# Optimization experiments

Measured on AMD Instinct MI355X. Metric: run time of the kernel, lower is better.

The kernel has to match this reference:

```python
import jax, jax.numpy as jnp
import numpy as np

DIM = 192
NUM_HEADS = 6
WIN = (2, 7, 7)


def _relative_position_index(win):
    d, h, w = win
    coords = np.stack(np.meshgrid(np.arange(d), np.arange(h), np.arange(w), indexing='ij'))
    cf = coords.reshape(3, -1)  # (3, n)
    rel = cf[:, :, None] - cf[:, None, :]  # (3, n, n)
    rel = rel.transpose(1, 2, 0).copy()
    rel[:, :, 0] += d - 1
    rel[:, :, 1] += h - 1
    rel[:, :, 2] += w - 1
    rel[:, :, 0] *= (2 * h - 1) * (2 * w - 1)
    rel[:, :, 1] *= 2 * w - 1
    return rel.sum(-1).astype(np.int32)  # (n, n)


def setup_inputs() -> dict:
    key = jax.random.key(0)
    ks = jax.random.split(key, 8)
    n = WIN[0] * WIN[1] * WIN[2]  # 98
    table_size = (2 * WIN[0] - 1) * (2 * WIN[1] - 1) * (2 * WIN[2] - 1)  # 507
    b_ = 4096
    nW = 64
    x = jax.random.normal(ks[0], (b_, n, DIM), dtype=jnp.float32)
    mask = jax.random.normal(ks[1], (nW, n, n), dtype=jnp.float32)
    qkv_w = jax.random.normal(ks[2], (3 * DIM, DIM), dtype=jnp.float32) * (DIM ** -0.5)
    qkv_b = jnp.zeros((3 * DIM,), dtype=jnp.float32)
    proj_w = jax.random.normal(ks[3], (DIM, DIM), dtype=jnp.float32) * (DIM ** -0.5)
    proj_b = jnp.zeros((DIM,), dtype=jnp.float32)
    rpb_table = jax.random.normal(ks[4], (table_size, NUM_HEADS), dtype=jnp.float32) * 0.02
    rel_idx = jnp.asarray(_relative_position_index(WIN))  # (n, n) int32
    return {"x": x, "mask": mask, "qkv_w": qkv_w, "qkv_b": qkv_b,
            "proj_w": proj_w, "proj_b": proj_b, "rpb_table": rpb_table,
            "rel_idx": rel_idx}


def reference(x, mask, qkv_w, qkv_b, proj_w, proj_b, rpb_table, rel_idx):
    b_, n, c = x.shape
    H = NUM_HEADS
    hd = c // H
    scale = hd ** -0.5
    # QKV projection: (b_, n, 3, H, hd) -> (3, b_, H, n, hd)
    qkv = (x @ qkv_w.T + qkv_b).reshape(b_, n, 3, H, hd).transpose(2, 0, 3, 1, 4)
    q, k, v = qkv[0] * scale, qkv[1], qkv[2]
    attn = jnp.einsum('bhnd,bhmd->bhnm', q, k)
    # relative position bias gathered per (n, n) pair -> (H, n, n)
    bias = rpb_table[rel_idx]  # (n, n, H)
    attn = attn + bias.transpose(2, 0, 1)[None]
    # window mask add
    nW = mask.shape[0]
    attn = attn.reshape(b_ // nW, nW, H, n, n) + mask[None, :, None]
    attn = attn.reshape(b_, H, n, n)
    attn = jax.nn.softmax(attn, axis=-1)
    out = jnp.einsum('bhnm,bhmd->bhnd', attn, v)
    out = out.transpose(0, 2, 1, 3).reshape(b_, n, c)
    return out @ proj_w.T + proj_b
```

## Files before the change

### kernel.cpp

```cpp
#include <hip/hip_runtime.h>
#include <hip/hip_bf16.h>

#define NN 98
#define CC 192
#define NH 6
#define HDIM 32
#define NWIN 64
#define MPAD 100
#define NSTR 200
#define SWS 1920

typedef float f32x4 __attribute__((ext_vector_type(4)));
typedef __bf16 bf16x8 __attribute__((ext_vector_type(8)));
typedef __bf16 bf16x4 __attribute__((ext_vector_type(4)));

__device__ __forceinline__ f32x4 mfma_bf16(bf16x8 a, bf16x8 b, f32x4 c) {
  return __builtin_amdgcn_mfma_f32_16x16x32_bf16(a, b, c, 0, 0, 0);
}

__device__ __forceinline__ bf16x8 zero8() {
  bf16x8 z;
#pragma unroll
  for (int i = 0; i < 8; ++i) z[i] = (__bf16)0.0f;
  return z;
}

__device__ __forceinline__ bf16x8 ldw8(const float* __restrict__ p) {
  f32x4 a = *(const f32x4*)p;
  f32x4 b = *(const f32x4*)(p + 4);
  bf16x8 r;
  r[0] = (__bf16)a[0]; r[1] = (__bf16)a[1]; r[2] = (__bf16)a[2]; r[3] = (__bf16)a[3];
  r[4] = (__bf16)b[0]; r[5] = (__bf16)b[1]; r[6] = (__bf16)b[2]; r[7] = (__bf16)b[3];
  return r;
}

__device__ __forceinline__ bf16x8 ldlds8(const __bf16* p, int row, int k0) {
  int rc = row < NN ? row : (NN - 1);
  bf16x8 v = *(const bf16x8*)(p + rc * NSTR + k0);
  if (row >= NN) v = zero8();
  return v;
}

__global__ void prep_kernel(const float* __restrict__ mask,
                            const float* __restrict__ rpb,
                            const int* __restrict__ rel_idx,
                            float* __restrict__ biasp,
                            float* __restrict__ maskp) {
  int i = blockIdx.x * 256 + threadIdx.x;
  if (i < NH * NN * MPAD) {
    int m = i % MPAD;
    int rem = i / MPAD;
    int n = rem % NN;
    int h = rem / NN;
    biasp[i] = (m < NN) ? rpb[rel_idx[n * NN + m] * NH + h] : -1e30f;
  }
  if (i < NWIN * NN * MPAD) {
    int m = i % MPAD;
    int rem = i / MPAD;
    int n = rem % NN;
    int wi = rem / NN;
    maskp[i] = (m < NN) ? mask[(wi * NN + n) * NN + m] : -1e30f;
  }
}

__global__ __launch_bounds__(384, 3) void attn_kernel(
    const float* __restrict__ x,
    const float* __restrict__ qkv_w,
    const float* __restrict__ qkv_b,
    const float* __restrict__ proj_w,
    const float* __restrict__ proj_b,
    const float* __restrict__ biasp,
    const float* __restrict__ maskp,
    float* __restrict__ out) {
  __shared__ alignas(16) __bf16 xs[NN * NSTR];
  __shared__ alignas(16) __bf16 stage[NH * SWS];

  const int b = blockIdx.x;
  const int tid = threadIdx.x;
  const int w = tid >> 6;
  const int lane = tid & 63;
  const int l15 = lane & 15;
  const int quad = lane >> 4;
  __bf16* st = stage + w * SWS;

  const float* xb = x + (size_t)b * (NN * CC);
  for (int i = tid; i < NN * CC / 4; i += 384) {
    int e = i * 4;
    int n = e / CC;
    int c = e - n * CC;
    f32x4 v = *(const f32x4*)(xb + e);
    bf16x4 p;
    p[0] = (__bf16)v[0]; p[1] = (__bf16)v[1]; p[2] = (__bf16)v[2]; p[3] = (__bf16)v[3];
    *(bf16x4*)&xs[n * NSTR + c] = p;
  }
  __syncthreads();

  f32x4 accA[4][7];
#pragma unroll
  for (int ct = 0; ct < 2; ++ct) {
    float bk = qkv_b[CC + w * HDIM + ct * 16 + l15];
    float bv = qkv_b[2 * CC + w * HDIM + ct * 16 + l15];
#pragma unroll
    for (int rt = 0; rt < 7; ++rt) {
      f32x4 tk = {bk, bk, bk, bk};
      f32x4 tv = {bv, bv, bv, bv};
      accA[ct][rt] = tk;
      accA[2 + ct][rt] = tv;
    }
  }
#pragma unroll
  for (int ks = 0; ks < 6; ++ks) {
    const int k0 = ks * 32 + quad * 8;
    bf16x8 b0 = ldw8(qkv_w + (size_t)(CC + w * HDIM + l15) * CC + k0);
    bf16x8 b1 = ldw8(qkv_w + (size_t)(CC + w * HDIM + 16 + l15) * CC + k0);
    bf16x8 b2 = ldw8(qkv_w + (size_t)(2 * CC + w * HDIM + l15) * CC + k0);
    bf16x8 b3 = ldw8(qkv_w + (size_t)(2 * CC + w * HDIM + 16 + l15) * CC + k0);
#pragma unroll
    for (int rt = 0; rt < 7; ++rt) {
      bf16x8 a = ldlds8(xs, rt * 16 + l15, k0);
      accA[0][rt] = mfma_bf16(a, b0, accA[0][rt]);
      accA[1][rt] = mfma_bf16(a, b1, accA[1][rt]);
      accA[2][rt] = mfma_bf16(a, b2, accA[2][rt]);
      accA[3][rt] = mfma_bf16(a, b3, accA[3][rt]);
    }
  }

  bf16x8 ka[7];
#pragma unroll
  for (int rt = 0; rt < 7; ++rt) {
#pragma unroll
    for (int ct = 0; ct < 2; ++ct) {
      f32x4 v = accA[ct][rt];
      int hd = ct * 16 + l15;
#pragma unroll
      for (int r = 0; r < 4; ++r) st[(quad * 4 + r) * 40 + hd] = (__bf16)v[r];
    }
    bf16x8 f = *(const bf16x8*)&st[l15 * 40 + quad * 8];
    if (rt * 16 + l15 >= NN) f = zero8();
    ka[rt] = f;
  }

  bf16x8 va[2][4];
#pragma unroll
  for (int ks = 0; ks < 4; ++ks) {
#pragma unroll
    for (int h2 = 0; h2 < 2; ++h2) {
      int rt = 2 * ks + h2;
      if (rt < 7) {
#pragma unroll
        for (int ct = 0; ct < 2; ++ct) {
          f32x4 v = accA[2 + ct][rt];
          int d = ct * 16 + l15;
          int mloc = h2 * 16 + quad * 4;
          bf16x4 p;
#pragma unroll
          for (int r = 0; r < 4; ++r) p[r] = (__bf16)v[r];
          *(bf16x4*)&st[d * 40 + mloc] = p;
        }
      }
    }
#pragma unroll
    for (int dt = 0; dt < 2; ++dt) {
      bf16x8 f = *(const bf16x8*)&st[(dt * 16 + l15) * 40 + quad * 8];
      if (ks == 3 && quad >= 2) f = zero8();
      va[dt][ks] = f;
    }
  }

  f32x4 accB[2][7];
#pragma unroll
  for (int ct = 0; ct < 2; ++ct) {
    float bq = qkv_b[w * HDIM + ct * 16 + l15];
#pragma unroll
    for (int rt = 0; rt < 7; ++rt) {
      f32x4 t = {bq, bq, bq, bq};
      accB[ct][rt] = t;
    }
  }
#pragma unroll
  for (int ks = 0; ks < 6; ++ks) {
    const int k0 = ks * 32 + quad * 8;
    bf16x8 b0 = ldw8(qkv_w + (size_t)(w * HDIM + l15) * CC + k0);
    bf16x8 b1 = ldw8(qkv_w + (size_t)(w * HDIM + 16 + l15) * CC + k0);
#pragma unroll
    for (int rt = 0; rt < 7; ++rt) {
      bf16x8 a = ldlds8(xs, rt * 16 + l15, k0);
      accB[0][rt] = mfma_bf16(a, b0, accB[0][rt]);
      accB[1][rt] = mfma_bf16(a, b1, accB[1][rt]);
    }
  }

  const float scale = 0.17677669529663687f;
  bf16x8 qb[7];
#pragma unroll
  for (int rt = 0; rt < 7; ++rt) {
#pragma unroll
    for (int ct = 0; ct < 2; ++ct) {
      f32x4 v = accB[ct][rt];
      int hd = ct * 16 + l15;
#pragma unroll
      for (int r = 0; r < 4; ++r) st[(quad * 4 + r) * 40 + hd] = (__bf16)(v[r] * scale);
    }
    bf16x8 f = *(const bf16x8*)&st[l15 * 40 + quad * 8];
    if (rt * 16 + l15 >= NN) f = zero8();
    qb[rt] = f;
  }

  __syncthreads();
  __bf16* O_lds = xs;

  const int wmask = b & (NWIN - 1);
#pragma unroll 1
  for (int nb = 0; nb < 7; ++nb) {
    f32x4 sacc[7];
    const f32x4 z4 = {0.f, 0.f, 0.f, 0.f};
#pragma unroll
    for (int mt = 0; mt < 7; ++mt) sacc[mt] = mfma_bf16(ka[mt], qb[nb], z4);

    int n = nb * 16 + l15;
    bool nvalid = (n < NN);
    int nc = nvalid ? n : 0;
    const float* bp = biasp + (size_t)(w * NN + nc) * MPAD;
    const float* mp = maskp + (size_t)(wmask * NN + nc) * MPAD;

    float sv[28];
    float mx = -3.0e38f;
#pragma unroll
    for (int mt = 0; mt < 7; ++mt) {
      int m0 = mt * 16 + quad * 4;
      f32x4 add = z4;
      bool ld = nvalid && (m0 < MPAD);
      if (ld) {
        f32x4 bm = *(const f32x4*)(bp + m0);
        f32x4 mm = *(const f32x4*)(mp + m0);
        add = bm + mm;
      }
#pragma unroll
      for (int r = 0; r < 4; ++r) {
        float v = ld ? (sacc[mt][r] + add[r]) : -1e30f;
        sv[mt * 4 + r] = v;
        mx = fmaxf(mx, v);
      }
    }
    mx = fmaxf(mx, __shfl_xor(mx, 16, 64));
    mx = fmaxf(mx, __shfl_xor(mx, 32, 64));
    float sum = 0.f;
#pragma unroll
    for (int i = 0; i < 28; ++i) {
      float p = __expf(sv[i] - mx);
      sv[i] = p;
      sum += p;
    }
    sum += __shfl_xor(sum, 16, 64);
    sum += __shfl_xor(sum, 32, 64);
    float rinv = 1.0f / sum;

#pragma unroll
    for (int mt = 0; mt < 7; ++mt) {
      bf16x4 p;
#pragma unroll
      for (int r = 0; r < 4; ++r) p[r] = (__bf16)sv[mt * 4 + r];
      *(bf16x4*)&st[l15 * 120 + mt * 16 + quad * 4] = p;
    }
    bf16x8 pf[4];
#pragma unroll
    for (int ks = 0; ks < 4; ++ks) {
      bf16x8 f = *(const bf16x8*)&st[l15 * 120 + ks * 32 + quad * 8];
      if (ks == 3 && quad >= 2) f = zero8();
      pf[ks] = f;
    }

#pragma unroll
    for (int dt = 0; dt < 2; ++dt) {
      f32x4 o = z4;
#pragma unroll
      for (int ks = 0; ks < 4; ++ks) o = mfma_bf16(va[dt][ks], pf[ks], o);
      if (nvalid) {
        bf16x4 p;
#pragma unroll
        for (int r = 0; r < 4; ++r) p[r] = (__bf16)(o[r] * rinv);
        *(bf16x4*)&O_lds[n * NSTR + w * HDIM + dt * 16 + quad * 4] = p;
      }
    }
  }
  __syncthreads();

  f32x4 accP[2][7];
#pragma unroll
  for (int ct = 0; ct < 2; ++ct) {
    float pb = proj_b[w * HDIM + ct * 16 + l15];
#pragma unroll
    for (int rt = 0; rt < 7; ++rt) {
      f32x4 t = {pb, pb, pb, pb};
      accP[ct][rt] = t;
    }
  }
#pragma unroll
  for (int ks = 0; ks < 6; ++ks) {
    const int k0 = ks * 32 + quad * 8;
    bf16x8 b0 = ldw8(proj_w + (size_t)(w * HDIM + l15) * CC + k0);
    bf16x8 b1 = ldw8(proj_w + (size_t)(w * HDIM + 16 + l15) * CC + k0);
#pragma unroll
    for (int rt = 0; rt < 7; ++rt) {
      bf16x8 a = ldlds8(O_lds, rt * 16 + l15, k0);
      accP[0][rt] = mfma_bf16(a, b0, accP[0][rt]);
      accP[1][rt] = mfma_bf16(a, b1, accP[1][rt]);
    }
  }

  float* ob = out + (size_t)b * (NN * CC);
#pragma unroll
  for (int ct = 0; ct < 2; ++ct) {
    int cout = w * HDIM + ct * 16 + l15;
#pragma unroll
    for (int rt = 0; rt < 7; ++rt) {
      f32x4 v = accP[ct][rt];
#pragma unroll
      for (int r = 0; r < 4; ++r) {
        int n = rt * 16 + quad * 4 + r;
        if (n < NN) ob[n * CC + cout] = v[r];
      }
    }
  }
}

extern "C" void kernel_launch(void* const* d_in, const int* in_sizes, int n_in,
                              void* d_out, int out_size, void* d_ws, size_t ws_size,
                              hipStream_t stream) {
  const float* x = (const float*)d_in[0];
  const float* mask = (const float*)d_in[1];
  const float* qkv_w = (const float*)d_in[2];
  const float* qkv_b = (const float*)d_in[3];
  const float* proj_w = (const float*)d_in[4];
  const float* proj_b = (const float*)d_in[5];
  const float* rpb = (const float*)d_in[6];
  const int* rel_idx = (const int*)d_in[7];

  float* biasp = (float*)d_ws;
  float* maskp = biasp + NH * NN * MPAD;

  int prep_threads = NWIN * NN * MPAD;
  prep_kernel<<<(prep_threads + 255) / 256, 256, 0, stream>>>(mask, rpb, rel_idx, biasp, maskp);
  attn_kernel<<<4096, 384, 0, stream>>>(x, qkv_w, qkv_b, proj_w, proj_b, biasp, maskp,
                                        (float*)d_out);
}
```

Baseline: 1.746 ms.

## Pre-convert weights to bf16 fragment layout, split K/V GEMMs, use exp2 softmax

The prep kernel now converts the QKV and projection weights once into bf16 arrays laid out in MFMA fragment order, so each lane loads one contiguous 16-byte vector instead of two fp32 vectors plus conversions in every block. The K and V projections are computed one after the other with a shared accumulator set, which lowers register pressure. Softmax switches to exp2, with log2(e) folded into the query scale, bias and mask. This adds work and workspace to the prep kernel and reloads the x tile from LDS one extra time.

```diff
diff --git a/kernel.cpp b/kernel.cpp
--- a/kernel.cpp
+++ b/kernel.cpp
@@ -10,6 +10,10 @@
 #define NSTR 200
 #define SWS 1920
 
+#define WKV_ELEMS 73728
+#define WQ_ELEMS  36864
+#define WP_ELEMS  36864
+
 typedef float f32x4 __attribute__((ext_vector_type(4)));
 typedef __bf16 bf16x8 __attribute__((ext_vector_type(8)));
 typedef __bf16 bf16x4 __attribute__((ext_vector_type(4)));
@@ -25,13 +29,12 @@
   return z;
 }
 
-__device__ __forceinline__ bf16x8 ldw8(const float* __restrict__ p) {
-  f32x4 a = *(const f32x4*)p;
-  f32x4 b = *(const f32x4*)(p + 4);
-  bf16x8 r;
-  r[0] = (__bf16)a[0]; r[1] = (__bf16)a[1]; r[2] = (__bf16)a[2]; r[3] = (__bf16)a[3];
-  r[4] = (__bf16)b[0]; r[5] = (__bf16)b[1]; r[6] = (__bf16)b[2]; r[7] = (__bf16)b[3];
-  return r;
+__device__ __forceinline__ float fast_exp2(float x) {
+#if __has_builtin(__builtin_amdgcn_exp2f)
+  return __builtin_amdgcn_exp2f(x);
+#else
+  return exp2f(x);
+#endif
 }
 
 __device__ __forceinline__ bf16x8 ldlds8(const __bf16* p, int row, int k0) {
@@ -44,33 +47,65 @@
 __global__ void prep_kernel(const float* __restrict__ mask,
                             const float* __restrict__ rpb,
                             const int* __restrict__ rel_idx,
+                            const float* __restrict__ qkv_w,
+                            const float* __restrict__ proj_w,
                             float* __restrict__ biasp,
-                            float* __restrict__ maskp) {
+                            float* __restrict__ maskp,
+                            __bf16* __restrict__ wkvp,
+                            __bf16* __restrict__ wqp,
+                            __bf16* __restrict__ wpp) {
+  const float LOG2E = 1.4426950408889634f;
   int i = blockIdx.x * 256 + threadIdx.x;
   if (i < NH * NN * MPAD) {
     int m = i % MPAD;
     int rem = i / MPAD;
     int n = rem % NN;
     int h = rem / NN;
-    biasp[i] = (m < NN) ? rpb[rel_idx[n * NN + m] * NH + h] : -1e30f;
+    biasp[i] = (m < NN) ? rpb[rel_idx[n * NN + m] * NH + h] * LOG2E : -1e30f;
   }
   if (i < NWIN * NN * MPAD) {
     int m = i % MPAD;
     int rem = i / MPAD;
     int n = rem % NN;
     int wi = rem / NN;
-    maskp[i] = (m < NN) ? mask[(wi * NN + n) * NN + m] : -1e30f;
+    maskp[i] = (m < NN) ? mask[(wi * NN + n) * NN + m] * LOG2E : -1e30f;
+  }
+  if (i < WKV_ELEMS) {
+    int j = i & 7;
+    int lane = (i >> 3) & 63;
+    int f = (i >> 9) & 3;
+    int t = i >> 11;
+    int ks = t % 6;
+    int w = t / 6;
+    int l15 = lane & 15, quad = lane >> 4;
+    int row = (f < 2 ? CC : 2 * CC) + w * HDIM + (f & 1) * 16 + l15;
+    int col = ks * 32 + quad * 8 + j;
+    wkvp[i] = (__bf16)qkv_w[row * CC + col];
+  }
+  if (i < WQ_ELEMS) {
+    int j = i & 7;
+    int lane = (i >> 3) & 63;
+    int f = (i >> 9) & 1;
+    int t = i >> 10;
+    int ks = t % 6;
+    int w = t / 6;
+    int l15 = lane & 15, quad = lane >> 4;
+    int row = w * HDIM + f * 16 + l15;
+    int col = ks * 32 + quad * 8 + j;
+    wqp[i] = (__bf16)qkv_w[row * CC + col];
+    wpp[i] = (__bf16)proj_w[row * CC + col];
   }
 }
 
 __global__ __launch_bounds__(384, 3) void attn_kernel(
     const float* __restrict__ x,
-    const float* __restrict__ qkv_w,
     const float* __restrict__ qkv_b,
-    const float* __restrict__ proj_w,
     const float* __restrict__ proj_b,
     const float* __restrict__ biasp,
     const float* __restrict__ maskp,
+    const __bf16* __restrict__ wkvp,
+    const __bf16* __restrict__ wqp,
+    const __bf16* __restrict__ wpp,
     float* __restrict__ out) {
   __shared__ alignas(16) __bf16 xs[NN * NSTR];
   __shared__ alignas(16) __bf16 stage[NH * SWS];
@@ -95,33 +130,27 @@
   }
   __syncthreads();
 
-  f32x4 accA[4][7];
+  f32x4 acc[2][7];
+
 #pragma unroll
   for (int ct = 0; ct < 2; ++ct) {
-    float bk = qkv_b[CC + w * HDIM + ct * 16 + l15];
-    float bv = qkv_b[2 * CC + w * HDIM + ct * 16 + l15];
-#pragma unroll
-    for (int rt = 0; rt < 7; ++rt) {
-      f32x4 tk = {bk, bk, bk, bk};
-      f32x4 tv = {bv, bv, bv, bv};
-      accA[ct][rt] = tk;
-      accA[2 + ct][rt] = tv;
-    }
-  }
-#pragma unroll
-  for (int ks = 0; ks < 6; ++ks) {
-    const int k0 = ks * 32 + quad * 8;
-    bf16x8 b0 = ldw8(qkv_w + (size_t)(CC + w * HDIM + l15) * CC + k0);
-    bf16x8 b1 = ldw8(qkv_w + (size_t)(CC + w * HDIM + 16 + l15) * CC + k0);
-    bf16x8 b2 = ldw8(qkv_w + (size_t)(2 * CC + w * HDIM + l15) * CC + k0);
-    bf16x8 b3 = ldw8(qkv_w + (size_t)(2 * CC + w * HDIM + 16 + l15) * CC + k0);
-#pragma unroll
-    for (int rt = 0; rt < 7; ++rt) {
-      bf16x8 a = ldlds8(xs, rt * 16 + l15, k0);
-      accA[0][rt] = mfma_bf16(a, b0, accA[0][rt]);
-      accA[1][rt] = mfma_bf16(a, b1, accA[1][rt]);
-      accA[2][rt] = mfma_bf16(a, b2, accA[2][rt]);
-      accA[3][rt] = mfma_bf16(a, b3, accA[3][rt]);
+    float bb = qkv_b[CC + w * HDIM + ct * 16 + l15];
+#pragma unroll
+    for (int rt = 0; rt < 7; ++rt) { f32x4 t = {bb, bb, bb, bb}; acc[ct][rt] = t; }
+  }
+  {
+    const __bf16* wb = wkvp + (size_t)(w * 24) * 512 + lane * 8;
+#pragma unroll
+    for (int ks = 0; ks < 6; ++ks) {
+      bf16x8 b0 = *(const bf16x8*)(wb + (ks * 4 + 0) * 512);
+      bf16x8 b1 = *(const bf16x8*)(wb + (ks * 4 + 1) * 512);
+      const int k0 = ks * 32 + quad * 8;
+#pragma unroll
+      for (int rt = 0; rt < 7; ++rt) {
+        bf16x8 a = ldlds8(xs, rt * 16 + l15, k0);
+        acc[0][rt] = mfma_bf16(a, b0, acc[0][rt]);
+        acc[1][rt] = mfma_bf16(a, b1, acc[1][rt]);
+      }
     }
   }
 
@@ -130,7 +159,7 @@
   for (int rt = 0; rt < 7; ++rt) {
 #pragma unroll
     for (int ct = 0; ct < 2; ++ct) {
-      f32x4 v = accA[ct][rt];
+      f32x4 v = acc[ct][rt];
       int hd = ct * 16 + l15;
 #pragma unroll
       for (int r = 0; r < 4; ++r) st[(quad * 4 + r) * 40 + hd] = (__bf16)v[r];
@@ -140,6 +169,28 @@
     ka[rt] = f;
   }
 
+#pragma unroll
+  for (int ct = 0; ct < 2; ++ct) {
+    float bb = qkv_b[2 * CC + w * HDIM + ct * 16 + l15];
+#pragma unroll
+    for (int rt = 0; rt < 7; ++rt) { f32x4 t = {bb, bb, bb, bb}; acc[ct][rt] = t; }
+  }
+  {
+    const __bf16* wb = wkvp + (size_t)(w * 24) * 512 + lane * 8;
+#pragma unroll
+    for (int ks = 0; ks < 6; ++ks) {
+      bf16x8 b0 = *(const bf16x8*)(wb + (ks * 4 + 2) * 512);
+      bf16x8 b1 = *(const bf16x8*)(wb + (ks * 4 + 3) * 512);
+      const int k0 = ks * 32 + quad * 8;
+#pragma unroll
+      for (int rt = 0; rt < 7; ++rt) {
+        bf16x8 a = ldlds8(xs, rt * 16 + l15, k0);
+        acc[0][rt] = mfma_bf16(a, b0, acc[0][rt]);
+        acc[1][rt] = mfma_bf16(a, b1, acc[1][rt]);
+      }
+    }
+  }
+
   bf16x8 va[2][4];
 #pragma unroll
   for (int ks = 0; ks < 4; ++ks) {
@@ -149,7 +200,7 @@
       if (rt < 7) {
 #pragma unroll
         for (int ct = 0; ct < 2; ++ct) {
-          f32x4 v = accA[2 + ct][rt];
+          f32x4 v = acc[ct][rt];
           int d = ct * 16 + l15;
           int mloc = h2 * 16 + quad * 4;
           bf16x4 p;
@@ -167,39 +218,38 @@
     }
   }
 
-  f32x4 accB[2][7];
 #pragma unroll
   for (int ct = 0; ct < 2; ++ct) {
     float bq = qkv_b[w * HDIM + ct * 16 + l15];
 #pragma unroll
-    for (int rt = 0; rt < 7; ++rt) {
-      f32x4 t = {bq, bq, bq, bq};
-      accB[ct][rt] = t;
-    }
-  }
-#pragma unroll
-  for (int ks = 0; ks < 6; ++ks) {
-    const int k0 = ks * 32 + quad * 8;
-    bf16x8 b0 = ldw8(qkv_w + (size_t)(w * HDIM + l15) * CC + k0);
-    bf16x8 b1 = ldw8(qkv_w + (size_t)(w * HDIM + 16 + l15) * CC + k0);
-#pragma unroll
-    for (int rt = 0; rt < 7; ++rt) {
-      bf16x8 a = ldlds8(xs, rt * 16 + l15, k0);
-      accB[0][rt] = mfma_bf16(a, b0, accB[0][rt]);
-      accB[1][rt] = mfma_bf16(a, b1, accB[1][rt]);
-    }
-  }
-
-  const float scale = 0.17677669529663687f;
+    for (int rt = 0; rt < 7; ++rt) { f32x4 t = {bq, bq, bq, bq}; acc[ct][rt] = t; }
+  }
+  {
+    const __bf16* wb = wqp + (size_t)(w * 12) * 512 + lane * 8;
+#pragma unroll
+    for (int ks = 0; ks < 6; ++ks) {
+      bf16x8 b0 = *(const bf16x8*)(wb + (ks * 2 + 0) * 512);
+      bf16x8 b1 = *(const bf16x8*)(wb + (ks * 2 + 1) * 512);
+      const int k0 = ks * 32 + quad * 8;
+#pragma unroll
+      for (int rt = 0; rt < 7; ++rt) {
+        bf16x8 a = ldlds8(xs, rt * 16 + l15, k0);
+        acc[0][rt] = mfma_bf16(a, b0, acc[0][rt]);
+        acc[1][rt] = mfma_bf16(a, b1, acc[1][rt]);
+      }
+    }
+  }
+
+  const float qscale = 0.17677669529663687f * 1.4426950408889634f;
   bf16x8 qb[7];
 #pragma unroll
   for (int rt = 0; rt < 7; ++rt) {
 #pragma unroll
     for (int ct = 0; ct < 2; ++ct) {
-      f32x4 v = accB[ct][rt];
+      f32x4 v = acc[ct][rt];
       int hd = ct * 16 + l15;
 #pragma unroll
-      for (int r = 0; r < 4; ++r) st[(quad * 4 + r) * 40 + hd] = (__bf16)(v[r] * scale);
+      for (int r = 0; r < 4; ++r) st[(quad * 4 + r) * 40 + hd] = (__bf16)(v[r] * qscale);
     }
     bf16x8 f = *(const bf16x8*)&st[l15 * 40 + quad * 8];
     if (rt * 16 + l15 >= NN) f = zero8();
@@ -212,8 +262,8 @@
   const int wmask = b & (NWIN - 1);
 #pragma unroll 1
   for (int nb = 0; nb < 7; ++nb) {
+    const f32x4 z4 = {0.f, 0.f, 0.f, 0.f};
     f32x4 sacc[7];
-    const f32x4 z4 = {0.f, 0.f, 0.f, 0.f};
 #pragma unroll
     for (int mt = 0; mt < 7; ++mt) sacc[mt] = mfma_bf16(ka[mt], qb[nb], z4);
 
@@ -223,13 +273,12 @@
     const float* bp = biasp + (size_t)(w * NN + nc) * MPAD;
     const float* mp = maskp + (size_t)(wmask * NN + nc) * MPAD;
 
-    float sv[28];
     float mx = -3.0e38f;
 #pragma unroll
     for (int mt = 0; mt < 7; ++mt) {
       int m0 = mt * 16 + quad * 4;
+      bool ld = nvalid && (m0 < MPAD);
       f32x4 add = z4;
-      bool ld = nvalid && (m0 < MPAD);
       if (ld) {
         f32x4 bm = *(const f32x4*)(bp + m0);
         f32x4 mm = *(const f32x4*)(mp + m0);
@@ -238,7 +287,7 @@
 #pragma unroll
       for (int r = 0; r < 4; ++r) {
         float v = ld ? (sacc[mt][r] + add[r]) : -1e30f;
-        sv[mt * 4 + r] = v;
+        sacc[mt][r] = v;
         mx = fmaxf(mx, v);
       }
     }
@@ -246,10 +295,13 @@
     mx = fmaxf(mx, __shfl_xor(mx, 32, 64));
     float sum = 0.f;
 #pragma unroll
-    for (int i = 0; i < 28; ++i) {
-      float p = __expf(sv[i] - mx);
-      sv[i] = p;
-      sum += p;
+    for (int mt = 0; mt < 7; ++mt) {
+#pragma unroll
+      for (int r = 0; r < 4; ++r) {
+        float p = fast_exp2(sacc[mt][r] - mx);
+        sacc[mt][r] = p;
+        sum += p;
+      }
     }
     sum += __shfl_xor(sum, 16, 64);
     sum += __shfl_xor(sum, 32, 64);
@@ -259,7 +311,7 @@
     for (int mt = 0; mt < 7; ++mt) {
       bf16x4 p;
 #pragma unroll
-      for (int r = 0; r < 4; ++r) p[r] = (__bf16)sv[mt * 4 + r];
+      for (int r = 0; r < 4; ++r) p[r] = (__bf16)sacc[mt][r];
       *(bf16x4*)&st[l15 * 120 + mt * 16 + quad * 4] = p;
     }
     bf16x8 pf[4];
@@ -290,21 +342,21 @@
   for (int ct = 0; ct < 2; ++ct) {
     float pb = proj_b[w * HDIM + ct * 16 + l15];
 #pragma unroll
-    for (int rt = 0; rt < 7; ++rt) {
-      f32x4 t = {pb, pb, pb, pb};
-      accP[ct][rt] = t;
-    }
-  }
-#pragma unroll
-  for (int ks = 0; ks < 6; ++ks) {
-    const int k0 = ks * 32 + quad * 8;
-    bf16x8 b0 = ldw8(proj_w + (size_t)(w * HDIM + l15) * CC + k0);
-    bf16x8 b1 = ldw8(proj_w + (size_t)(w * HDIM + 16 + l15) * CC + k0);
-#pragma unroll
-    for (int rt = 0; rt < 7; ++rt) {
-      bf16x8 a = ldlds8(O_lds, rt * 16 + l15, k0);
-      accP[0][rt] = mfma_bf16(a, b0, accP[0][rt]);
-      accP[1][rt] = mfma_bf16(a, b1, accP[1][rt]);
+    for (int rt = 0; rt < 7; ++rt) { f32x4 t = {pb, pb, pb, pb}; accP[ct][rt] = t; }
+  }
+  {
+    const __bf16* wb = wpp + (size_t)(w * 12) * 512 + lane * 8;
+#pragma unroll
+    for (int ks = 0; ks < 6; ++ks) {
+      bf16x8 b0 = *(const bf16x8*)(wb + (ks * 2 + 0) * 512);
+      bf16x8 b1 = *(const bf16x8*)(wb + (ks * 2 + 1) * 512);
+      const int k0 = ks * 32 + quad * 8;
+#pragma unroll
+      for (int rt = 0; rt < 7; ++rt) {
+        bf16x8 a = ldlds8(O_lds, rt * 16 + l15, k0);
+        accP[0][rt] = mfma_bf16(a, b0, accP[0][rt]);
+        accP[1][rt] = mfma_bf16(a, b1, accP[1][rt]);
+      }
     }
   }
 
@@ -338,9 +390,13 @@
 
   float* biasp = (float*)d_ws;
   float* maskp = biasp + NH * NN * MPAD;
+  __bf16* wkvp = (__bf16*)(maskp + NWIN * NN * MPAD);
+  __bf16* wqp = wkvp + WKV_ELEMS;
+  __bf16* wpp = wqp + WQ_ELEMS;
 
   int prep_threads = NWIN * NN * MPAD;
-  prep_kernel<<<(prep_threads + 255) / 256, 256, 0, stream>>>(mask, rpb, rel_idx, biasp, maskp);
-  attn_kernel<<<4096, 384, 0, stream>>>(x, qkv_w, qkv_b, proj_w, proj_b, biasp, maskp,
-                                        (float*)d_out);
-}
+  prep_kernel<<<(prep_threads + 255) / 256, 256, 0, stream>>>(
+      mask, rpb, rel_idx, qkv_w, proj_w, biasp, maskp, wkvp, wqp, wpp);
+  attn_kernel<<<4096, 384, 0, stream>>>(x, qkv_b, proj_b, biasp, maskp,
+                                        wkvp, wqp, wpp, (float*)d_out);
+}
```

After: 1.562 ms. -10.5%, faster.
